# Performance work log

Hardware: AMD Instinct MI355X
Metric: run time of the kernel (lower is better)

The kernel has to match this reference:

```python
import jax, jax.numpy as jnp
import numpy as np

V, E, H, B, S = 50257, 1024, 1024, 32, 1024

def setup_inputs() -> dict:
    key = jax.random.key(0)
    ks = jax.random.split(key, 16)
    s = 0.02
    return {
        "word_inputs": jax.random.randint(ks[0], (B, 1), 0, V),
        "hidden": jax.random.normal(ks[1], (1, B, H), jnp.float32),
        "output_encoder": jax.random.normal(ks[2], (B, S, H), jnp.float32),
        "emb": jax.random.normal(ks[3], (V, E), jnp.float32) * 0.2,
        "W_a1": jax.random.normal(ks[4], (H, 2 * H), jnp.float32) * s,
        "b_a1": jnp.zeros((H,), jnp.float32),
        "W_a2": jax.random.normal(ks[5], (1, H), jnp.float32) * s,
        "b_a2": jnp.zeros((1,), jnp.float32),
        "W_c": jax.random.normal(ks[6], (H, 2 * H), jnp.float32) * s,
        "b_c": jnp.zeros((H,), jnp.float32),
        "W_ih": jax.random.normal(ks[7], (3 * H, E), jnp.float32) * s,
        "W_hh": jax.random.normal(ks[8], (3 * H, H), jnp.float32) * s,
        "b_ih": jnp.zeros((3 * H,), jnp.float32),
        "b_hh": jnp.zeros((3 * H,), jnp.float32),
        "W_fc": jax.random.normal(ks[9], (V, H), jnp.float32) * 0.2,
        "b_fc": jnp.zeros((V,), jnp.float32),
    }

def reference(word_inputs, hidden, output_encoder, emb, W_a1, b_a1, W_a2, b_a2,
              W_c, b_c, W_ih, W_hh, b_ih, b_hh, W_fc, b_fc):
    b, s, h = output_encoder.shape
    h_prev = hidden[0]                                      # [B,H]
    # Bahdanau additive attention, vectorized over all S timesteps
    eh = jnp.concatenate(
        [output_encoder, jnp.broadcast_to(h_prev[:, None, :], (b, s, h))],
        axis=-1)                                            # [B,S,2H]
    scores = jnp.tanh(jnp.einsum('bsk,hk->bsh', eh, W_a1) + b_a1)
    scores = (jnp.einsum('bsh,oh->bso', scores, W_a2) + b_a2)[..., 0]  # [B,S]
    attn = jax.nn.softmax(scores, axis=1)                   # [B,S]
    context = jnp.einsum('bs,bsh->bh', attn, output_encoder)  # [B,H]
    embedded = emb[word_inputs.reshape(-1)]                 # [B,E]
    ec = jnp.concatenate([embedded, context], axis=-1)      # [B,E+H]
    x = jax.nn.relu(ec @ W_c.T + b_c)                       # [B,H]
    # single-step GRU (PyTorch gate order: r, z, n)
    gi = x @ W_ih.T + b_ih                                  # [B,3H]
    gh = h_prev @ W_hh.T + b_hh                             # [B,3H]
    i_r, i_z, i_n = jnp.split(gi, 3, axis=-1)
    h_r, h_z, h_n = jnp.split(gh, 3, axis=-1)
    r = jax.nn.sigmoid(i_r + h_r)
    z = jax.nn.sigmoid(i_z + h_z)
    n = jnp.tanh(i_n + r * h_n)
    h_new = (1.0 - z) * n + z * h_prev                      # [B,H]
    out = jax.nn.relu(h_new) @ W_fc.T + b_fc                # [B,V]
    return out, h_new[None, :, :]
```

## Files before the change

### kernel.cpp

```cpp
#include <hip/hip_runtime.h>

#define B_  32
#define S_  1024
#define H_  1024
#define V_  50257

typedef __attribute__((ext_vector_type(8))) short bf16x8;
typedef __attribute__((ext_vector_type(4))) float f32x4;
typedef __attribute__((ext_vector_type(8))) unsigned short u16x8;

__device__ __forceinline__ unsigned short f2b(float f) {
  union { float f; unsigned u; } v; v.f = f;
  unsigned r = 0x7FFFu + ((v.u >> 16) & 1u);
  return (unsigned short)((v.u + r) >> 16);
}
__device__ __forceinline__ float b2f(unsigned short h) {
  union { unsigned u; float f; } v; v.u = ((unsigned)h) << 16;
  return v.f;
}

__device__ __forceinline__ void async16(void* lds, const void* g) {
  typedef __attribute__((address_space(3))) void as3_void;
  typedef __attribute__((address_space(1))) void as1_void;
  as3_void* l = (as3_void*)(unsigned)(unsigned long long)lds;
  const as1_void* s = (const as1_void*)(unsigned long long)g;
  __builtin_amdgcn_global_load_lds(s, l, 16, 0, 0);
}

__global__ void conv_f32_bf16(const float* __restrict__ src, unsigned short* __restrict__ dst) {
  size_t i = ((size_t)blockIdx.x * 256 + threadIdx.x) * 8;
  float4 v0 = *(const float4*)(src + i);
  float4 v1 = *(const float4*)(src + i + 4);
  u16x8 o;
  o[0]=f2b(v0.x); o[1]=f2b(v0.y); o[2]=f2b(v0.z); o[3]=f2b(v0.w);
  o[4]=f2b(v1.x); o[5]=f2b(v1.y); o[6]=f2b(v1.z); o[7]=f2b(v1.w);
  *(u16x8*)(dst + i) = o;
}

__global__ void conv_wa1(const float* __restrict__ wa1, unsigned short* __restrict__ dst) {
  size_t i = ((size_t)blockIdx.x * 256 + threadIdx.x) * 8;
  int h = (int)(i >> 10), k = (int)(i & 1023);
  const float* s = wa1 + (size_t)h * 2048 + k;
  float4 v0 = *(const float4*)(s);
  float4 v1 = *(const float4*)(s + 4);
  u16x8 o;
  o[0]=f2b(v0.x); o[1]=f2b(v0.y); o[2]=f2b(v0.z); o[3]=f2b(v0.w);
  o[4]=f2b(v1.x); o[5]=f2b(v1.y); o[6]=f2b(v1.z); o[7]=f2b(v1.w);
  *(u16x8*)(dst + i) = o;
}

__global__ void part2_kernel(const float* __restrict__ wa1, const float* __restrict__ hidden,
                             const float* __restrict__ b_a1, float* __restrict__ part2) {
  int h = blockIdx.x;
  __shared__ float wrow[H_];
  for (int i = threadIdx.x; i < H_; i += 256) wrow[i] = wa1[(size_t)h * 2048 + 1024 + i];
  __syncthreads();
  int wave = threadIdx.x >> 6, lane = threadIdx.x & 63;
  float bias = b_a1[h];
  for (int bb = 0; bb < 8; ++bb) {
    int b = wave * 8 + bb;
    float acc = 0.f;
    for (int k = lane; k < H_; k += 64) acc += wrow[k] * hidden[b * H_ + k];
    #pragma unroll
    for (int off = 32; off; off >>= 1) acc += __shfl_xor(acc, off);
    if (lane == 0) part2[b * H_ + h] = acc + bias;
  }
}

#define NT_ 16
#define BAR()  __builtin_amdgcn_s_barrier()
#define SB0()  __builtin_amdgcn_sched_barrier(0)
#define VM6()  asm volatile("s_waitcnt vmcnt(6)" ::: "memory")
#define VM0()  asm volatile("s_waitcnt vmcnt(0)" ::: "memory")

#define LOADA(MH) { _Pragma("unroll") for (int m_ = 0; m_ < 4; ++m_) \
  { _Pragma("unroll") for (int ks_ = 0; ks_ < 2; ++ks_) { \
    int r_ = wr*128 + (MH)*64 + m_*16 + l15; \
    int lin_ = ks_*16384 + r_*64 + l16*16; \
    int sw_ = lin_ ^ (((lin_>>9)&1)<<5); \
    af[m_][ks_] = *(const bf16x8*)(smem + buf*32768 + sw_); } } }

#define LOADB() { _Pragma("unroll") for (int n_ = 0; n_ < 4; ++n_) \
  { _Pragma("unroll") for (int ks_ = 0; ks_ < 2; ++ks_) { \
    int r_ = wc*64 + n_*16 + l15; \
    int lin_ = ks_*16384 + r_*64 + l16*16; \
    int sw_ = lin_ ^ (((lin_>>9)&1)<<5); \
    bfr[n_][ks_] = *(const bf16x8*)(smem + 65536 + buf*32768 + sw_); } } }

#define QUAD(MH, NH) { _Pragma("unroll") for (int m_ = 0; m_ < 4; ++m_) \
  { _Pragma("unroll") for (int n_ = 0; n_ < 2; ++n_) { \
    acc[(MH)*4+m_][(NH)*2+n_] = __builtin_amdgcn_mfma_f32_16x16x32_bf16(af[m_][0], bfr[(NH)*2+n_][0], acc[(MH)*4+m_][(NH)*2+n_], 0,0,0); \
    acc[(MH)*4+m_][(NH)*2+n_] = __builtin_amdgcn_mfma_f32_16x16x32_bf16(af[m_][1], bfr[(NH)*2+n_][1], acc[(MH)*4+m_][(NH)*2+n_], 0,0,0); } } }

#define PHASES(T, DO_B1, DO_T2, VMOP) { \
  const int buf = (T) & 1; \
  LOADA(0); LOADB(); \
  if (DO_B1) stB((T)+1, 1, buf^1); \
  BAR(); SB0(); \
  __builtin_amdgcn_s_setprio(1); QUAD(0,0); __builtin_amdgcn_s_setprio(0); \
  SB0(); BAR(); \
  if (DO_T2) stB((T)+2, 0, buf); \
  BAR(); SB0(); \
  __builtin_amdgcn_s_setprio(1); QUAD(0,1); __builtin_amdgcn_s_setprio(0); \
  SB0(); BAR(); \
  LOADA(1); \
  BAR(); SB0(); \
  __builtin_amdgcn_s_setprio(1); QUAD(1,1); __builtin_amdgcn_s_setprio(0); \
  SB0(); BAR(); \
  if (DO_T2) { stA((T)+2, 0, buf); stA((T)+2, 1, buf); } \
  VMOP; \
  BAR(); SB0(); \
  __builtin_amdgcn_s_setprio(1); QUAD(1,0); __builtin_amdgcn_s_setprio(0); \
  SB0(); BAR(); }

__global__ __launch_bounds__(512, 2) void scores_gemm8(
    const unsigned short* __restrict__ A,
    const unsigned short* __restrict__ Bm,
    const float* __restrict__ part2,
    const float* __restrict__ wa2,
    float* __restrict__ partials)
{
  extern __shared__ char smem[];
  const int tid = threadIdx.x;
  const int wave = tid >> 6, lane = tid & 63;
  const int wr = wave >> 2, wc = wave & 3;
  const int l15 = lane & 15, l16 = lane >> 4;
  const int bm = blockIdx.x, bn = blockIdx.y;

  const unsigned short* Abase = A  + (size_t)(bm * 256) * 1024;
  const unsigned short* Bbase = Bm + (size_t)(bn * 256) * 1024;

  const int Lc = tid * 16;
  const int Ls = Lc ^ (((Lc >> 9) & 1) << 5);
  const int sr = Ls >> 6;
  const int sk = (Ls >> 1) & 31;

  auto stA = [&](int t, int h, int db) {
    char* base = smem + db * 32768 + h * 8192 + Lc;
    const unsigned short* src = Abase + (size_t)(h * 128 + sr) * 1024 + t * 64 + sk;
    async16(base,         src);
    async16(base + 16384, src + 32);
  };
  auto stB = [&](int t, int h, int db) {
    char* base = smem + 65536 + db * 32768 + h * 8192 + Lc;
    const unsigned short* src = Bbase + (size_t)(h * 128 + sr) * 1024 + t * 64 + sk;
    async16(base,         src);
    async16(base + 16384, src + 32);
  };

  f32x4 acc[8][4];
  #pragma unroll
  for (int i = 0; i < 8; ++i)
    #pragma unroll
    for (int j = 0; j < 4; ++j) acc[i][j] = (f32x4){0.f, 0.f, 0.f, 0.f};
  bf16x8 af[4][2], bfr[4][2];

  stA(0, 0, 0); stA(0, 1, 0); stB(0, 0, 0); stB(0, 1, 0);
  stB(1, 0, 1); stA(1, 0, 1); stA(1, 1, 1);
  VM6();
  BAR();

  #pragma unroll 1
  for (int t = 0; t < NT_ - 2; ++t) PHASES(t, 1, 1, VM6());
  PHASES(NT_ - 2, 1, 0, VM0());
  PHASES(NT_ - 1, 0, 0, (void)0);

  const int b = bm >> 2;
  float w2[4], p2[4];
  #pragma unroll
  for (int ni = 0; ni < 4; ++ni) {
    int col = bn * 256 + wc * 64 + ni * 16 + l15;
    w2[ni] = wa2[col];
    p2[ni] = part2[b * H_ + col];
  }
  #pragma unroll
  for (int mi = 0; mi < 8; ++mi) {
    #pragma unroll
    for (int r = 0; r < 4; ++r) {
      float s = 0.f;
      #pragma unroll
      for (int ni = 0; ni < 4; ++ni)
        s += w2[ni] * tanhf(acc[mi][ni][r] + p2[ni]);
      s += __shfl_xor(s, 1); s += __shfl_xor(s, 2);
      s += __shfl_xor(s, 4); s += __shfl_xor(s, 8);
      if (l15 == 0) {
        int row = bm * 256 + wr * 128 + mi * 16 + l16 * 4 + r;
        partials[(size_t)row * 16 + bn * 4 + wc] = s;
      }
    }
  }
}

__global__ void softmax_kernel(const float* __restrict__ partials, const float* __restrict__ b_a2,
                               float* __restrict__ attn) {
  int b = blockIdx.x, s = threadIdx.x;
  int lane = s & 63, wid = s >> 6;
  const float4* p = (const float4*)(partials + (size_t)(b * S_ + s) * 16);
  float sc = b_a2[0];
  #pragma unroll
  for (int i = 0; i < 4; ++i) { float4 v = p[i]; sc += v.x + v.y + v.z + v.w; }
  __shared__ float rmax[16], rsum[16];
  float m = sc;
  #pragma unroll
  for (int off = 32; off; off >>= 1) m = fmaxf(m, __shfl_xor(m, off));
  if (lane == 0) rmax[wid] = m;
  __syncthreads();
  float M = rmax[0];
  #pragma unroll
  for (int i = 1; i < 16; ++i) M = fmaxf(M, rmax[i]);
  float e = expf(sc - M);
  float su = e;
  #pragma unroll
  for (int off = 32; off; off >>= 1) su += __shfl_xor(su, off);
  if (lane == 0) rsum[wid] = su;
  __syncthreads();
  float T = 0.f;
  #pragma unroll
  for (int i = 0; i < 16; ++i) T += rsum[i];
  attn[b * S_ + s] = e / T;
}

__global__ void ctx_partial_kernel(const unsigned short* __restrict__ encbf,
                                   const float* __restrict__ attn, float* __restrict__ ctxp) {
  int sc = blockIdx.x, b = blockIdx.y, t = threadIdx.x;
  int h4 = t * 4;
  float a0 = 0, a1 = 0, a2 = 0, a3 = 0;
  const unsigned short* base = encbf + (size_t)b * S_ * H_ + h4;
  const float* aw = attn + b * S_ + sc * 64;
  #pragma unroll 4
  for (int i = 0; i < 64; ++i) {
    float w = aw[i];
    ushort4 ev = *(const ushort4*)(base + (size_t)(sc * 64 + i) * H_);
    a0 += w * b2f(ev.x); a1 += w * b2f(ev.y); a2 += w * b2f(ev.z); a3 += w * b2f(ev.w);
  }
  float4 o = {a0, a1, a2, a3};
  *(float4*)(ctxp + (size_t)(sc * B_ + b) * H_ + h4) = o;
}

__global__ void prep_kernel(const float* __restrict__ ctxp, const float* __restrict__ emb,
                            const int* __restrict__ word, const float* __restrict__ hidden,
                            unsigned short* __restrict__ ec_bf, unsigned short* __restrict__ hprev_bf) {
  int b = blockIdx.x;
  int w = word[b];
  for (int h = threadIdx.x; h < H_; h += 256) {
    float c = 0.f;
    #pragma unroll
    for (int sc = 0; sc < 16; ++sc) c += ctxp[(size_t)(sc * B_ + b) * H_ + h];
    ec_bf[b * 2048 + 1024 + h] = f2b(c);
    ec_bf[b * 2048 + h] = f2b(emb[(size_t)w * H_ + h]);
    hprev_bf[b * H_ + h] = f2b(hidden[b * H_ + h]);
  }
}

__global__ __launch_bounds__(256) void skinny_gemm(
    const unsigned short* __restrict__ A, const float* __restrict__ Bw,
    float* __restrict__ C, const float* __restrict__ bias,
    int N, int K, int KC, int ldc, int mode)
{
  int n0 = blockIdx.x * 64;
  int kc = blockIdx.y;
  int wave = threadIdx.x >> 6, lane = threadIdx.x & 63;
  int l15 = lane & 15, l16 = lane >> 4;
  int col = n0 + wave * 16 + l15;
  int vclamp = col < N ? col : N - 1;
  const unsigned short* a0p = A + l15 * K + l16 * 8;
  const unsigned short* a1p = A + (16 + l15) * K + l16 * 8;
  const float* bp = Bw + (size_t)vclamp * K + l16 * 8;
  f32x4 acc0 = {0.f, 0.f, 0.f, 0.f}, acc1 = {0.f, 0.f, 0.f, 0.f};
  int k0 = kc * KC, k1 = (k0 + KC < K) ? (k0 + KC) : K;
  #pragma unroll 4
  for (int k = k0; k < k1; k += 32) {
    bf16x8 a0 = *(const bf16x8*)(a0p + k);
    bf16x8 a1 = *(const bf16x8*)(a1p + k);
    float4 bv0 = *(const float4*)(bp + k);
    float4 bv1 = *(const float4*)(bp + k + 4);
    bf16x8 bb;
    bb[0] = (short)f2b(bv0.x); bb[1] = (short)f2b(bv0.y);
    bb[2] = (short)f2b(bv0.z); bb[3] = (short)f2b(bv0.w);
    bb[4] = (short)f2b(bv1.x); bb[5] = (short)f2b(bv1.y);
    bb[6] = (short)f2b(bv1.z); bb[7] = (short)f2b(bv1.w);
    acc0 = __builtin_amdgcn_mfma_f32_16x16x32_bf16(a0, bb, acc0, 0, 0, 0);
    acc1 = __builtin_amdgcn_mfma_f32_16x16x32_bf16(a1, bb, acc1, 0, 0, 0);
  }
  if (col < N) {
    #pragma unroll
    for (int r = 0; r < 4; ++r) {
      int m = l16 * 4 + r;
      if (mode == 1) {
        float bv = bias[col];
        C[(size_t)m * ldc + col] = acc0[r] + bv;
        C[(size_t)(16 + m) * ldc + col] = acc1[r] + bv;
      } else {
        C[(size_t)(kc * 32 + m) * N + col] = acc0[r];
        C[(size_t)(kc * 32 + 16 + m) * N + col] = acc1[r];
      }
    }
  }
}

__global__ void xfinish_kernel(const float* __restrict__ xp, const float* __restrict__ b_c,
                               unsigned short* __restrict__ x_bf) {
  int i = blockIdx.x * 256 + threadIdx.x;
  int b = i >> 10, h = i & 1023;
  float v = b_c[h];
  #pragma unroll
  for (int kc = 0; kc < 16; ++kc) v += xp[(size_t)(kc * B_ + b) * H_ + h];
  x_bf[i] = f2b(v > 0.f ? v : 0.f);
}

__global__ void gates_kernel(const float* __restrict__ gip, const float* __restrict__ ghp,
                             const float* __restrict__ b_ih, const float* __restrict__ b_hh,
                             const float* __restrict__ hidden, float* __restrict__ hnew_out,
                             unsigned short* __restrict__ hr_bf) {
  int i = blockIdx.x * 256 + threadIdx.x;
  int b = i >> 10, h = i & 1023;
  float g[6];
  #pragma unroll
  for (int t = 0; t < 3; ++t) {
    int j = h + t * H_;
    float vi = b_ih[j], vh = b_hh[j];
    #pragma unroll
    for (int kc = 0; kc < 8; ++kc) {
      vi += gip[(size_t)(kc * B_ + b) * 3072 + j];
      vh += ghp[(size_t)(kc * B_ + b) * 3072 + j];
    }
    g[t] = vi; g[3 + t] = vh;
  }
  float r = 1.f / (1.f + expf(-(g[0] + g[3])));
  float z = 1.f / (1.f + expf(-(g[1] + g[4])));
  float n = tanhf(g[2] + r * g[5]);
  float hv = (1.f - z) * n + z * hidden[i];
  hnew_out[i] = hv;
  hr_bf[i] = f2b(hv > 0.f ? hv : 0.f);
}

extern "C" void kernel_launch(void* const* d_in, const int* in_sizes, int n_in,
                              void* d_out, int out_size, void* d_ws, size_t ws_size,
                              hipStream_t stream) {
  const int*   word   = (const int*)  d_in[0];
  const float* hidden = (const float*)d_in[1];
  const float* enc    = (const float*)d_in[2];
  const float* emb    = (const float*)d_in[3];
  const float* W_a1   = (const float*)d_in[4];
  const float* b_a1   = (const float*)d_in[5];
  const float* W_a2   = (const float*)d_in[6];
  const float* b_a2   = (const float*)d_in[7];
  const float* W_c    = (const float*)d_in[8];
  const float* b_c    = (const float*)d_in[9];
  const float* W_ih   = (const float*)d_in[10];
  const float* W_hh   = (const float*)d_in[11];
  const float* b_ih   = (const float*)d_in[12];
  const float* b_hh   = (const float*)d_in[13];
  const float* W_fc   = (const float*)d_in[14];
  const float* b_fc   = (const float*)d_in[15];
  float* out = (float*)d_out;

  if (ws_size < 71892992ull) return;

  char* ws = (char*)d_ws;
  unsigned short* enc_bf   = (unsigned short*)(ws + 0);
  float*          gip      = (float*)         (ws + 0);
  float*          ghp      = (float*)         (ws + 3145728);
  unsigned short* wa1_bf   = (unsigned short*)(ws + 67108864);
  float*          xp       = (float*)         (ws + 67108864);
  float*          part2    = (float*)         (ws + 69206016);
  float*          partials = (float*)         (ws + 69337088);
  float*          ctxp     = (float*)         (ws + 69337088);
  float*          attn     = (float*)         (ws + 71434240);
  unsigned short* ec_bf    = (unsigned short*)(ws + 71565312);
  unsigned short* hprev_bf = (unsigned short*)(ws + 71696384);
  unsigned short* x_bf     = (unsigned short*)(ws + 71761920);
  unsigned short* hr_bf    = (unsigned short*)(ws + 71827456);

  hipFuncSetAttribute((const void*)scores_gemm8,
                      hipFuncAttributeMaxDynamicSharedMemorySize, 131072);

  conv_f32_bf16<<<dim3(16384), dim3(256), 0, stream>>>(enc, enc_bf);
  conv_wa1<<<dim3(512), dim3(256), 0, stream>>>(W_a1, wa1_bf);
  part2_kernel<<<dim3(1024), dim3(256), 0, stream>>>(W_a1, hidden, b_a1, part2);
  scores_gemm8<<<dim3(128, 4), dim3(512), 131072, stream>>>(enc_bf, wa1_bf, part2, W_a2, partials);
  softmax_kernel<<<dim3(32), dim3(1024), 0, stream>>>(partials, b_a2, attn);
  ctx_partial_kernel<<<dim3(16, 32), dim3(256), 0, stream>>>(enc_bf, attn, ctxp);
  prep_kernel<<<dim3(32), dim3(256), 0, stream>>>(ctxp, emb, word, hidden, ec_bf, hprev_bf);
  skinny_gemm<<<dim3(16, 16), dim3(256), 0, stream>>>(ec_bf, W_c, xp, (const float*)nullptr,
                                                      1024, 2048, 128, 0, 0);
  xfinish_kernel<<<dim3(128), dim3(256), 0, stream>>>(xp, b_c, x_bf);
  skinny_gemm<<<dim3(48, 8), dim3(256), 0, stream>>>(x_bf, W_ih, gip, (const float*)nullptr,
                                                     3072, 1024, 128, 0, 0);
  skinny_gemm<<<dim3(48, 8), dim3(256), 0, stream>>>(hprev_bf, W_hh, ghp, (const float*)nullptr,
                                                     3072, 1024, 128, 0, 0);
  gates_kernel<<<dim3(128), dim3(256), 0, stream>>>(gip, ghp, b_ih, b_hh, hidden,
                                                    out + (size_t)B_ * V_, hr_bf);
  skinny_gemm<<<dim3(786, 1), dim3(256), 0, stream>>>(hr_bf, W_fc, out, b_fc,
                                                      V_, 1024, 1024, V_, 1);
}
```

Baseline: 291.3 us.

## Fuse W_a1 prep kernels, batch GRU GEMMs, and re-layout scores GEMM LDS tiles

```diff
diff --git a/kernel.cpp b/kernel.cpp
--- a/kernel.cpp
+++ b/kernel.cpp
@@ -37,25 +37,26 @@
   *(u16x8*)(dst + i) = o;
 }
 
-__global__ void conv_wa1(const float* __restrict__ wa1, unsigned short* __restrict__ dst) {
-  size_t i = ((size_t)blockIdx.x * 256 + threadIdx.x) * 8;
-  int h = (int)(i >> 10), k = (int)(i & 1023);
-  const float* s = wa1 + (size_t)h * 2048 + k;
-  float4 v0 = *(const float4*)(s);
-  float4 v1 = *(const float4*)(s + 4);
-  u16x8 o;
-  o[0]=f2b(v0.x); o[1]=f2b(v0.y); o[2]=f2b(v0.z); o[3]=f2b(v0.w);
-  o[4]=f2b(v1.x); o[5]=f2b(v1.y); o[6]=f2b(v1.z); o[7]=f2b(v1.w);
-  *(u16x8*)(dst + i) = o;
-}
-
-__global__ void part2_kernel(const float* __restrict__ wa1, const float* __restrict__ hidden,
-                             const float* __restrict__ b_a1, float* __restrict__ part2) {
+__global__ void wa1_prep_kernel(const float* __restrict__ wa1, const float* __restrict__ hidden,
+                                const float* __restrict__ b_a1,
+                                unsigned short* __restrict__ wa1_bf, float* __restrict__ part2) {
   int h = blockIdx.x;
+  int tid = threadIdx.x;
+  {
+    int c = tid * 4;
+    float4 v = *(const float4*)(wa1 + (size_t)h * 2048 + c);
+    ushort4 o;
+    o.x = f2b(v.x); o.y = f2b(v.y); o.z = f2b(v.z); o.w = f2b(v.w);
+    *(ushort4*)(wa1_bf + (size_t)h * 1024 + c) = o;
+  }
   __shared__ float wrow[H_];
-  for (int i = threadIdx.x; i < H_; i += 256) wrow[i] = wa1[(size_t)h * 2048 + 1024 + i];
+  {
+    int c = tid * 4;
+    float4 v = *(const float4*)(wa1 + (size_t)h * 2048 + 1024 + c);
+    wrow[c] = v.x; wrow[c+1] = v.y; wrow[c+2] = v.z; wrow[c+3] = v.w;
+  }
   __syncthreads();
-  int wave = threadIdx.x >> 6, lane = threadIdx.x & 63;
+  int wave = tid >> 6, lane = tid & 63;
   float bias = b_a1[h];
   for (int bb = 0; bb < 8; ++bb) {
     int b = wave * 8 + bb;
@@ -75,17 +76,17 @@
 
 #define LOADA(MH) { _Pragma("unroll") for (int m_ = 0; m_ < 4; ++m_) \
   { _Pragma("unroll") for (int ks_ = 0; ks_ < 2; ++ks_) { \
-    int r_ = wr*128 + (MH)*64 + m_*16 + l15; \
-    int lin_ = ks_*16384 + r_*64 + l16*16; \
+    int lr_ = (MH)*64 + m_*16 + l15; \
+    int lin_ = lr_*128 + ks_*64 + l16*16; \
     int sw_ = lin_ ^ (((lin_>>9)&1)<<5); \
-    af[m_][ks_] = *(const bf16x8*)(smem + buf*32768 + sw_); } } }
+    af[m_][ks_] = *(const bf16x8*)(smem + buf*32768 + wr*16384 + sw_); } } }
 
 #define LOADB() { _Pragma("unroll") for (int n_ = 0; n_ < 4; ++n_) \
   { _Pragma("unroll") for (int ks_ = 0; ks_ < 2; ++ks_) { \
-    int r_ = wc*64 + n_*16 + l15; \
-    int lin_ = ks_*16384 + r_*64 + l16*16; \
+    int lr_ = (wc&1)*64 + n_*16 + l15; \
+    int lin_ = lr_*128 + ks_*64 + l16*16; \
     int sw_ = lin_ ^ (((lin_>>9)&1)<<5); \
-    bfr[n_][ks_] = *(const bf16x8*)(smem + 65536 + buf*32768 + sw_); } } }
+    bfr[n_][ks_] = *(const bf16x8*)(smem + 65536 + buf*32768 + (wc>>1)*16384 + sw_); } } }
 
 #define QUAD(MH, NH) { _Pragma("unroll") for (int m_ = 0; m_ < 4; ++m_) \
   { _Pragma("unroll") for (int n_ = 0; n_ < 2; ++n_) { \
@@ -132,20 +133,20 @@
 
   const int Lc = tid * 16;
   const int Ls = Lc ^ (((Lc >> 9) & 1) << 5);
-  const int sr = Ls >> 6;
-  const int sk = (Ls >> 1) & 31;
+  const int sr = Ls >> 7;
+  const int sk = (Ls & 127) >> 1;
 
   auto stA = [&](int t, int h, int db) {
-    char* base = smem + db * 32768 + h * 8192 + Lc;
+    char* dst = smem + db * 32768 + h * 16384 + Lc;
     const unsigned short* src = Abase + (size_t)(h * 128 + sr) * 1024 + t * 64 + sk;
-    async16(base,         src);
-    async16(base + 16384, src + 32);
+    async16(dst,        src);
+    async16(dst + 8192, src + 64 * 1024);
   };
   auto stB = [&](int t, int h, int db) {
-    char* base = smem + 65536 + db * 32768 + h * 8192 + Lc;
+    char* dst = smem + 65536 + db * 32768 + h * 16384 + Lc;
     const unsigned short* src = Bbase + (size_t)(h * 128 + sr) * 1024 + t * 64 + sk;
-    async16(base,         src);
-    async16(base + 16384, src + 32);
+    async16(dst,        src);
+    async16(dst + 8192, src + 64 * 1024);
   };
 
   f32x4 acc[8][4];
@@ -298,6 +299,47 @@
   }
 }
 
+__global__ __launch_bounds__(256) void ihhh_gemm(
+    const unsigned short* __restrict__ x_bf, const unsigned short* __restrict__ hprev_bf,
+    const float* __restrict__ W_ih, const float* __restrict__ W_hh,
+    float* __restrict__ gip, float* __restrict__ ghp)
+{
+  const unsigned short* A = blockIdx.z ? hprev_bf : x_bf;
+  const float* Bw = blockIdx.z ? W_hh : W_ih;
+  float* C = blockIdx.z ? ghp : gip;
+  const int N = 3072, K = 1024, KC = 128;
+  int n0 = blockIdx.x * 64;
+  int kc = blockIdx.y;
+  int wave = threadIdx.x >> 6, lane = threadIdx.x & 63;
+  int l15 = lane & 15, l16 = lane >> 4;
+  int col = n0 + wave * 16 + l15;
+  const unsigned short* a0p = A + l15 * K + l16 * 8;
+  const unsigned short* a1p = A + (16 + l15) * K + l16 * 8;
+  const float* bp = Bw + (size_t)col * K + l16 * 8;
+  f32x4 acc0 = {0.f, 0.f, 0.f, 0.f}, acc1 = {0.f, 0.f, 0.f, 0.f};
+  int k0 = kc * KC;
+  #pragma unroll 4
+  for (int k = k0; k < k0 + KC; k += 32) {
+    bf16x8 a0 = *(const bf16x8*)(a0p + k);
+    bf16x8 a1 = *(const bf16x8*)(a1p + k);
+    float4 bv0 = *(const float4*)(bp + k);
+    float4 bv1 = *(const float4*)(bp + k + 4);
+    bf16x8 bb;
+    bb[0] = (short)f2b(bv0.x); bb[1] = (short)f2b(bv0.y);
+    bb[2] = (short)f2b(bv0.z); bb[3] = (short)f2b(bv0.w);
+    bb[4] = (short)f2b(bv1.x); bb[5] = (short)f2b(bv1.y);
+    bb[6] = (short)f2b(bv1.z); bb[7] = (short)f2b(bv1.w);
+    acc0 = __builtin_amdgcn_mfma_f32_16x16x32_bf16(a0, bb, acc0, 0, 0, 0);
+    acc1 = __builtin_amdgcn_mfma_f32_16x16x32_bf16(a1, bb, acc1, 0, 0, 0);
+  }
+  #pragma unroll
+  for (int r = 0; r < 4; ++r) {
+    int m = l16 * 4 + r;
+    C[(size_t)(kc * 32 + m) * N + col] = acc0[r];
+    C[(size_t)(kc * 32 + 16 + m) * N + col] = acc1[r];
+  }
+}
+
 __global__ void xfinish_kernel(const float* __restrict__ xp, const float* __restrict__ b_c,
                                unsigned short* __restrict__ x_bf) {
   int i = blockIdx.x * 256 + threadIdx.x;
@@ -376,8 +418,7 @@
                       hipFuncAttributeMaxDynamicSharedMemorySize, 131072);
 
   conv_f32_bf16<<<dim3(16384), dim3(256), 0, stream>>>(enc, enc_bf);
-  conv_wa1<<<dim3(512), dim3(256), 0, stream>>>(W_a1, wa1_bf);
-  part2_kernel<<<dim3(1024), dim3(256), 0, stream>>>(W_a1, hidden, b_a1, part2);
+  wa1_prep_kernel<<<dim3(1024), dim3(256), 0, stream>>>(W_a1, hidden, b_a1, wa1_bf, part2);
   scores_gemm8<<<dim3(128, 4), dim3(512), 131072, stream>>>(enc_bf, wa1_bf, part2, W_a2, partials);
   softmax_kernel<<<dim3(32), dim3(1024), 0, stream>>>(partials, b_a2, attn);
   ctx_partial_kernel<<<dim3(16, 32), dim3(256), 0, stream>>>(enc_bf, attn, ctxp);
@@ -385,10 +426,7 @@
   skinny_gemm<<<dim3(16, 16), dim3(256), 0, stream>>>(ec_bf, W_c, xp, (const float*)nullptr,
                                                       1024, 2048, 128, 0, 0);
   xfinish_kernel<<<dim3(128), dim3(256), 0, stream>>>(xp, b_c, x_bf);
-  skinny_gemm<<<dim3(48, 8), dim3(256), 0, stream>>>(x_bf, W_ih, gip, (const float*)nullptr,
-                                                     3072, 1024, 128, 0, 0);
-  skinny_gemm<<<dim3(48, 8), dim3(256), 0, stream>>>(hprev_bf, W_hh, ghp, (const float*)nullptr,
-                                                     3072, 1024, 128, 0, 0);
+  ihhh_gemm<<<dim3(48, 8, 2), dim3(256), 0, stream>>>(x_bf, hprev_bf, W_ih, W_hh, gip, ghp);
   gates_kernel<<<dim3(128), dim3(256), 0, stream>>>(gip, ghp, b_ih, b_hh, hidden,
                                                     out + (size_t)B_ * V_, hr_bf);
   skinny_gemm<<<dim3(786, 1), dim3(256), 0, stream>>>(hr_bf, W_fc, out, b_fc,
```

Result: no change. 288.2 us (-1.1%).
